# Kernel optimization log

Measured on AMD Instinct MI355X. Metric: run time of the kernel, lower is better.

The kernel has to match this reference:

```python
import jax, jax.numpy as jnp
import numpy as np

B, S, D, H, DQK, DV, DFF, L = 8, 512, 512, 8, 64, 64, 2048, 2
SCALE = float(np.sqrt(DQK))


def sinusoid_pe(s, d):
    pos = jnp.arange(s, dtype=jnp.float32)[:, None]
    div = jnp.exp(jnp.arange(0, d, 2, dtype=jnp.float32) * (-np.log(10000.0) / d))
    pe = jnp.zeros((s, d), jnp.float32)
    pe = pe.at[:, 0::2].set(jnp.sin(pos * div))
    pe = pe.at[:, 1::2].set(jnp.cos(pos * div))
    return pe


def ms_masks(s, steps=(4, 8, 16), rep=2):
    # Vectorized equivalent of multi_scale_mask: window of `step` neighbors,
    # shifted near the boundaries so the total neighbor count stays = step.
    i = jnp.arange(s)[:, None]
    j = jnp.arange(s)[None, :]
    ms = []
    for step in steps:
        s2 = step // 2
        left = jnp.where(i < s // 2, jnp.minimum(i, s2), step - jnp.minimum(s - 1 - i, s2))
        right = step - left
        m = (j >= i - left) & (j <= i + right)
        ms += [m] * rep
    return jnp.stack(ms)  # [6, S, S] bool


def layer_norm(x, g, b):
    mu = x.mean(-1, keepdims=True)
    var = ((x - mu) ** 2).mean(-1, keepdims=True)
    return (x - mu) / jnp.sqrt(var + 1e-6) * g + b


def mha(qin, kin, vin, wq, wk, wv, wo, g, b, mask):
    bq, lq, _ = qin.shape
    lk = kin.shape[1]
    q = (qin @ wq).reshape(bq, lq, H, DQK).transpose(0, 2, 1, 3)  # bhqd
    k = (kin @ wk).reshape(bq, lk, H, DQK).transpose(0, 2, 1, 3)
    v = (vin @ wv).reshape(bq, lk, H, DV).transpose(0, 2, 1, 3)
    scores = jnp.einsum('bhqd,bhkd->bhqk', q / SCALE, k)
    scores = jnp.where(mask, scores, jnp.float32(-1e9))
    p = jax.nn.softmax(scores, axis=-1)
    o = jnp.einsum('bhqk,bhkd->bhqd', p, v).transpose(0, 2, 1, 3).reshape(bq, lq, H * DV)
    return layer_norm(o @ wo + qin, g, b)


def ffn(x, w1, b1, w2, b2, g, bb):
    h = jax.nn.relu(x @ w1 + b1)
    return layer_norm(h @ w2 + b2 + x, g, bb)


def setup_inputs() -> dict:
    key = jax.random.key(0)
    ks = jax.random.split(key, 40)
    it = iter(range(40))
    d = {}
    d['src_seq'] = jax.random.normal(ks[next(it)], (B, S, D), jnp.float32)
    d['trg_seq'] = jax.random.normal(ks[next(it)], (B, S, D), jnp.float32)
    d['enc_pad_num'] = jax.random.randint(ks[next(it)], (B,), 0, 64)
    d['dec_pad_num'] = jax.random.randint(ks[next(it)], (B,), 0, 64)

    def w(shape):
        return jax.random.normal(ks[next(it)], shape, jnp.float32) * 0.02

    for p in ('e_wq', 'e_wk', 'e_wv'):
        d[p] = w((L, D, H * DQK))
    d['e_wo'] = w((L, H * DV, D))
    d['e_g1'] = jnp.ones((L, D)); d['e_b1'] = jnp.zeros((L, D))
    d['e_w1'] = w((L, D, DFF)); d['e_bb1'] = jnp.zeros((L, DFF))
    d['e_w2'] = w((L, DFF, D)); d['e_bb2'] = jnp.zeros((L, D))
    d['e_g2'] = jnp.ones((L, D)); d['e_b2'] = jnp.zeros((L, D))
    for p in ('d_swq', 'd_swk', 'd_swv'):
        d[p] = w((L, D, H * DQK))
    d['d_swo'] = w((L, H * DV, D))
    d['d_g1'] = jnp.ones((L, D)); d['d_b1'] = jnp.zeros((L, D))
    for p in ('d_cwq', 'd_cwk', 'd_cwv'):
        d[p] = w((L, D, H * DQK))
    d['d_cwo'] = w((L, H * DV, D))
    d['d_g2'] = jnp.ones((L, D)); d['d_b2'] = jnp.zeros((L, D))
    d['d_w1'] = w((L, D, DFF)); d['d_bb1'] = jnp.zeros((L, DFF))
    d['d_w2'] = w((L, DFF, D)); d['d_bb2'] = jnp.zeros((L, D))
    d['d_g3'] = jnp.ones((L, D)); d['d_b3'] = jnp.zeros((L, D))
    return d


def reference(src_seq, trg_seq, enc_pad_num, dec_pad_num,
              e_wq, e_wk, e_wv, e_wo, e_g1, e_b1, e_w1, e_bb1, e_w2, e_bb2, e_g2, e_b2,
              d_swq, d_swk, d_swv, d_swo, d_g1, d_b1,
              d_cwq, d_cwk, d_cwv, d_cwo, d_g2, d_b2,
              d_w1, d_bb1, d_w2, d_bb2, d_g3, d_b3):
    ms = ms_masks(S)  # [6, S, S]
    src_pad = jnp.arange(S)[None, :] < (S - enc_pad_num)[:, None]  # [B, S]
    trg_pad = jnp.arange(S)[None, :] < (S - dec_pad_num)[:, None]

    def full_mask(pad):
        base = pad[:, None, None, :]  # [B,1,1,S]
        win = jnp.logical_and(ms[None], base)  # [B,6,S,S]
        dense = jnp.broadcast_to(base, (B, H - ms.shape[0], S, S))
        return jnp.concatenate([win, dense], axis=1)  # [B,H,S,S]

    src_mask = full_mask(src_pad)
    trg_mask = full_mask(trg_pad)
    pe = sinusoid_pe(S, D)

    x = src_seq + pe[None]
    for l in range(L):
        x = mha(x, x, x, e_wq[l], e_wk[l], e_wv[l], e_wo[l], e_g1[l], e_b1[l], src_mask)
        x = ffn(x, e_w1[l], e_bb1[l], e_w2[l], e_bb2[l], e_g2[l], e_b2[l])

    y = trg_seq + pe[None]
    for l in range(L):
        y = mha(y, y, y, d_swq[l], d_swk[l], d_swv[l], d_swo[l], d_g1[l], d_b1[l], trg_mask)
        y = mha(y, x, x, d_cwq[l], d_cwk[l], d_cwv[l], d_cwo[l], d_g2[l], d_b2[l], src_mask)
        y = ffn(y, d_w1[l], d_bb1[l], d_w2[l], d_bb2[l], d_g3[l], d_b3[l])
    return y
```

## Files before the change

kernel.cpp:

```cpp
#include <hip/hip_runtime.h>
#include <hip/hip_bf16.h>

#define BB 8
#define SS 512
#define DD 512
#define HH 8
#define DQKv 64
#define DFFv 2048
#define LL 2

typedef __attribute__((ext_vector_type(8))) __bf16 bf16x8;
typedef __attribute__((ext_vector_type(4))) float f32x4;

static __device__ __forceinline__ ushort f2b(float x) {
    unsigned int u = __float_as_uint(x);
    unsigned int r = (u + 0x7FFFu + ((u >> 16) & 1u)) >> 16;
    return (ushort)r;
}
static __device__ __forceinline__ float b2f(ushort u) {
    return __uint_as_float(((unsigned int)u) << 16);
}

typedef __attribute__((address_space(1))) const unsigned int gas_u32;
typedef __attribute__((address_space(3))) unsigned int las_u32;
static __device__ __forceinline__ void gload16(const void* g, void* l) {
    __builtin_amdgcn_global_load_lds((gas_u32*)g, (las_u32*)l, 16, 0, 0);
}

#define VMCNT4 asm volatile("s_waitcnt vmcnt(4)" ::: "memory")
#define VMCNT6 asm volatile("s_waitcnt vmcnt(6)" ::: "memory")
#define VMCNT0 asm volatile("s_waitcnt vmcnt(0)" ::: "memory")
#define LGKM0  asm volatile("s_waitcnt lgkmcnt(0)" ::: "memory")
#define SCHEDB __builtin_amdgcn_sched_barrier(0)
#define SBAR   __builtin_amdgcn_s_barrier()

__global__ __launch_bounds__(256) void add_pe2_k(const float* __restrict__ src,
                                                 const float* __restrict__ trg,
                                                 float* __restrict__ xf,
                                                 ushort* __restrict__ xb,
                                                 float* __restrict__ yf,
                                                 ushort* __restrict__ yb) {
    const int NQ = BB * SS * DD / 4;
    int i = blockIdx.x * 256 + threadIdx.x;
    const bool second = i >= NQ;
    const int ii = second ? i - NQ : i;
    const int rem = ii & (SS * DD / 4 - 1);
    const int d4 = rem & (DD / 4 - 1);
    const int s = rem >> 7;

    float4 a = ((const float4*)(second ? trg : src))[ii];
    const float c = -9.210340371976184f / 512.0f;
    const float div0 = __expf((float)(4 * d4) * c);
    const float div1 = __expf((float)(4 * d4 + 2) * c);
    const float a0 = (float)s * div0, a1 = (float)s * div1;
    a.x += sinf(a0); a.y += cosf(a0);
    a.z += sinf(a1); a.w += cosf(a1);

    float* of = second ? yf : xf;
    ushort* ob = second ? yb : xb;
    ((float4*)of)[ii] = a;
    ushort4 ub;
    ub.x = f2b(a.x); ub.y = f2b(a.y); ub.z = f2b(a.z); ub.w = f2b(a.w);
    ((ushort4*)ob)[ii] = ub;
}

__global__ __launch_bounds__(256) void tcast_k(const float* __restrict__ s0,
                                               const float* __restrict__ s1,
                                               const float* __restrict__ s2,
                                               const float* __restrict__ s3,
                                               ushort* __restrict__ dst,
                                               int K, int N) {
    __shared__ ushort st[64][72];
    const float* src = (blockIdx.z == 0) ? s0 : (blockIdx.z == 1) ? s1
                     : (blockIdx.z == 2) ? s2 : s3;
    ushort* d = dst + (size_t)blockIdx.z * K * N;
    const int k0 = blockIdx.y * 64, n0 = blockIdx.x * 64;
    const int t = threadIdx.x;
    const int r = t >> 2, c4 = (t & 3) * 16;
#pragma unroll
    for (int i = 0; i < 16; i += 4) {
        float4 v = *(const float4*)&src[(size_t)(k0 + r) * N + n0 + c4 + i];
        st[c4 + i + 0][r] = f2b(v.x);
        st[c4 + i + 1][r] = f2b(v.y);
        st[c4 + i + 2][r] = f2b(v.z);
        st[c4 + i + 3][r] = f2b(v.w);
    }
    __syncthreads();
    const int n = t >> 2, seg = (t & 3) * 16;
    *(uint4*)&d[(size_t)(n0 + n) * K + k0 + seg]     = *(const uint4*)&st[n][seg];
    *(uint4*)&d[(size_t)(n0 + n) * K + k0 + seg + 8] = *(const uint4*)&st[n][seg + 8];
}

#define NW 32
struct WTab {
    const float* src[NW];
    unsigned off[NW];
    int Kd[NW];
    int Nd[NW];
    int cum[NW + 1];
};

__global__ __launch_bounds__(256) void tcast_all_k(WTab tab, ushort* __restrict__ dst) {
    __shared__ ushort st[64][72];
    const int t = blockIdx.x;
    int m = 0;
    while (t >= tab.cum[m + 1]) ++m;
    const int local = t - tab.cum[m];
    const int ntx = tab.Nd[m];
    const int bx = local % ntx, by = local / ntx;
    const float* src = tab.src[m];
    ushort* d = dst + tab.off[m];
    const int N = ntx * 64, K = tab.Kd[m] * 64;
    const int k0 = by * 64, n0 = bx * 64;

    const int tt = threadIdx.x;
    const int r = tt >> 2, c4 = (tt & 3) * 16;
#pragma unroll
    for (int i = 0; i < 16; i += 4) {
        float4 v = *(const float4*)&src[(size_t)(k0 + r) * N + n0 + c4 + i];
        st[c4 + i + 0][r] = f2b(v.x);
        st[c4 + i + 1][r] = f2b(v.y);
        st[c4 + i + 2][r] = f2b(v.z);
        st[c4 + i + 3][r] = f2b(v.w);
    }
    __syncthreads();
    const int n = tt >> 2, seg = (tt & 3) * 16;
    *(uint4*)&d[(size_t)(n0 + n) * K + k0 + seg]     = *(const uint4*)&st[n][seg];
    *(uint4*)&d[(size_t)(n0 + n) * K + k0 + seg + 8] = *(const uint4*)&st[n][seg + 8];
}

template <bool BIAS, bool RES, bool RELU, bool OUTBF>
__global__ __launch_bounds__(256) void gemm2_k(const ushort* __restrict__ A,
                                               const ushort* __restrict__ Bt,
                                               const float* __restrict__ bias,
                                               const float* __restrict__ res,
                                               void* __restrict__ Cout,
                                               int M, int N, int K, int nbx) {
    __shared__ ushort sA[3][64 * 64];
    __shared__ ushort sB[3][64 * 64];

    const int tid = threadIdx.x;
    const int nwg = gridDim.x;
    const int wg = blockIdx.x;
    const int swz = (wg & 7) * (nwg >> 3) + (wg >> 3);
    const int bx = swz % nbx, by = swz / nbx;

    const int lane = tid & 63, w = tid >> 6;
    const int wm = w >> 1, wn = w & 1;
    const int llo = lane & 15, lhi = lane >> 4;

    const int srow = tid >> 3;
    const int scol = (((tid & 7) ^ (srow & 7)) * 8);
    const ushort* Ab = A + (size_t)(by * 64 + srow) * K + scol;
    const ushort* Bb = Bt + (size_t)(bx * 64 + srow) * K + scol;
    const int sOff = srow * 128 + (tid & 7) * 16;

    f32x4 acc[2][2] = {};
    const int nt = K >> 6;

#pragma unroll
    for (int i = 0; i < 2; ++i) {
        gload16(Ab + (size_t)i * 32 * K, (char*)sA[0] + sOff + i * 32 * 128);
        gload16(Bb + (size_t)i * 32 * K, (char*)sB[0] + sOff + i * 32 * 128);
    }
    if (nt > 1) {
#pragma unroll
        for (int i = 0; i < 2; ++i) {
            gload16(Ab + (size_t)i * 32 * K + 64, (char*)sA[1] + sOff + i * 32 * 128);
            gload16(Bb + (size_t)i * 32 * K + 64, (char*)sB[1] + sOff + i * 32 * 128);
        }
    }
    SCHEDB;

    for (int t = 0; t < nt; ++t) {
        if (t + 1 < nt) { VMCNT4; } else { VMCNT0; }
        LGKM0;
        SCHEDB;
        SBAR;
        SCHEDB;
        if (t + 2 < nt) {
            const int k0 = (t + 2) << 6;
            char* dA = (char*)sA[(t + 2) % 3] + sOff;
            char* dB = (char*)sB[(t + 2) % 3] + sOff;
#pragma unroll
            for (int i = 0; i < 2; ++i) {
                gload16(Ab + (size_t)i * 32 * K + k0, dA + i * 32 * 128);
                gload16(Bb + (size_t)i * 32 * K + k0, dB + i * 32 * 128);
            }
        }
        SCHEDB;
        const ushort* cA = sA[t % 3];
        const ushort* cB = sB[t % 3];
        const int sw = llo & 7;
#pragma unroll
        for (int ks = 0; ks < 2; ++ks) {
            const int pc = ((ks * 4 + lhi) ^ sw) * 8;
            bf16x8 af[2];
#pragma unroll
            for (int fa = 0; fa < 2; ++fa)
                af[fa] = *(const bf16x8*)&cA[(wm * 32 + fa * 16 + llo) * 64 + pc];
            bf16x8 bfrag[2];
#pragma unroll
            for (int fb = 0; fb < 2; ++fb)
                bfrag[fb] = *(const bf16x8*)&cB[(wn * 32 + fb * 16 + llo) * 64 + pc];
#pragma unroll
            for (int fa = 0; fa < 2; ++fa)
#pragma unroll
                for (int fb = 0; fb < 2; ++fb)
                    acc[fa][fb] = __builtin_amdgcn_mfma_f32_16x16x32_bf16(
                        af[fa], bfrag[fb], acc[fa][fb], 0, 0, 0);
        }
    }

#pragma unroll
    for (int fa = 0; fa < 2; ++fa) {
#pragma unroll
        for (int fb = 0; fb < 2; ++fb) {
            const int col = bx * 64 + wn * 32 + fb * 16 + llo;
            const float bv = BIAS ? bias[col] : 0.f;
#pragma unroll
            for (int j = 0; j < 4; ++j) {
                const int row = by * 64 + wm * 32 + fa * 16 + lhi * 4 + j;
                float v = acc[fa][fb][j] + bv;
                if (RES) v += res[(size_t)row * N + col];
                if (RELU) v = fmaxf(v, 0.f);
                if (OUTBF) ((ushort*)Cout)[(size_t)row * N + col] = f2b(v);
                else       ((float*)Cout)[(size_t)row * N + col] = v;
            }
        }
    }
}

template <bool BIAS, bool RES, bool RELU, bool OUTBF>
__global__ __launch_bounds__(256) void gemm3_k(const ushort* __restrict__ A,
                                               const ushort* __restrict__ Bt,
                                               const float* __restrict__ bias,
                                               const float* __restrict__ res,
                                               void* __restrict__ Cout,
                                               int M, int N, int K, int nbx) {
    __shared__ ushort sA[2][64 * 64];
    __shared__ ushort sB[2][128 * 64];

    const int tid = threadIdx.x;
    const int nwg = gridDim.x;
    const int wg = blockIdx.x;
    const int swz = (wg & 7) * (nwg >> 3) + (wg >> 3);
    const int bx = swz % nbx, by = swz / nbx;

    const int lane = tid & 63, w = tid >> 6;
    const int wm = w >> 1, wn = w & 1;
    const int llo = lane & 15, lhi = lane >> 4;

    const int srow = tid >> 3;
    const int scol = (((tid & 7) ^ (srow & 7)) * 8);
    const ushort* Ab = A + (size_t)(by * 64 + srow) * K + scol;
    const ushort* Bb = Bt + (size_t)(bx * 128 + srow) * K + scol;
    const int sOff = srow * 128 + (tid & 7) * 16;

    f32x4 acc[2][4] = {};
    const int nt = K >> 6;

#pragma unroll
    for (int i = 0; i < 2; ++i)
        gload16(Ab + (size_t)i * 32 * K, (char*)sA[0] + sOff + i * 32 * 128);
#pragma unroll
    for (int i = 0; i < 4; ++i)
        gload16(Bb + (size_t)i * 32 * K, (char*)sB[0] + sOff + i * 32 * 128);
    SCHEDB;

    for (int t = 0; t < nt; ++t) {
        if (t + 1 < nt) {
            const int k0 = (t + 1) << 6;
            char* dA = (char*)sA[(t + 1) & 1] + sOff;
            char* dB = (char*)sB[(t + 1) & 1] + sOff;
#pragma unroll
            for (int i = 0; i < 2; ++i)
                gload16(Ab + (size_t)i * 32 * K + k0, dA + i * 32 * 128);
#pragma unroll
            for (int i = 0; i < 4; ++i)
                gload16(Bb + (size_t)i * 32 * K + k0, dB + i * 32 * 128);
            SCHEDB;
            VMCNT6;
        } else {
            VMCNT0;
        }
        SCHEDB;
        SBAR;
        SCHEDB;
        const ushort* cA = sA[t & 1];
        const ushort* cB = sB[t & 1];
        const int sw = llo & 7;
#pragma unroll
        for (int ks = 0; ks < 2; ++ks) {
            const int pc = ((ks * 4 + lhi) ^ sw) * 8;
            bf16x8 af[2];
#pragma unroll
            for (int fa = 0; fa < 2; ++fa)
                af[fa] = *(const bf16x8*)&cA[(wm * 32 + fa * 16 + llo) * 64 + pc];
            bf16x8 bfrag[4];
#pragma unroll
            for (int fb = 0; fb < 4; ++fb)
                bfrag[fb] = *(const bf16x8*)&cB[(wn * 64 + fb * 16 + llo) * 64 + pc];
#pragma unroll
            for (int fa = 0; fa < 2; ++fa)
#pragma unroll
                for (int fb = 0; fb < 4; ++fb)
                    acc[fa][fb] = __builtin_amdgcn_mfma_f32_16x16x32_bf16(
                        af[fa], bfrag[fb], acc[fa][fb], 0, 0, 0);
        }
        LGKM0;
        SCHEDB;
        SBAR;
    }

#pragma unroll
    for (int fa = 0; fa < 2; ++fa) {
#pragma unroll
        for (int fb = 0; fb < 4; ++fb) {
            const int col = bx * 128 + wn * 64 + fb * 16 + llo;
            const float bv = BIAS ? bias[col] : 0.f;
#pragma unroll
            for (int j = 0; j < 4; ++j) {
                const int row = by * 64 + wm * 32 + fa * 16 + lhi * 4 + j;
                float v = acc[fa][fb][j] + bv;
                if (RES) v += res[(size_t)row * N + col];
                if (RELU) v = fmaxf(v, 0.f);
                if (OUTBF) ((ushort*)Cout)[(size_t)row * N + col] = f2b(v);
                else       ((float*)Cout)[(size_t)row * N + col] = v;
            }
        }
    }
}

__global__ __launch_bounds__(256) void attn_k(const ushort* __restrict__ QKV,
                                              ushort* __restrict__ O,
                                              const int* __restrict__ pad) {
    __shared__ ushort sQ[64][72];
    __shared__ ushort sK[64][72];
    __shared__ ushort sVt[64][72];
    __shared__ ushort sP[64][72];

    const int tid = threadIdx.x;
    const int b = blockIdx.z, h = blockIdx.y, q0 = blockIdx.x << 6;
    const int klim = SS - pad[b];
    const int lane = tid & 63, w = tid >> 6;
    const int qw0 = w << 4;
    const int lhi = lane >> 4, llo = lane & 15;
    const int ST = 3 * DD;

    {
        const int r = tid >> 2, seg = (tid & 3) << 4;
        const ushort* src = &QKV[(size_t)(b * SS + q0 + r) * ST + h * DQKv + seg];
        *(uint4*)&sQ[r][seg]     = *(const uint4*)src;
        *(uint4*)&sQ[r][seg + 8] = *(const uint4*)(src + 8);
    }

    auto window = [&](int i, int& wlo, int& whi) {
        if (h < 6) {
            const int step = 4 << (h >> 1);
            const int s2 = step >> 1;
            const int a1 = (i < s2) ? i : s2;
            const int a2 = ((SS - 1 - i) < s2) ? (SS - 1 - i) : s2;
            const int left = (i < SS / 2) ? a1 : (step - a2);
            wlo = i - left;
            whi = wlo + step;
        } else {
            wlo = 0;
            whi = SS - 1;
        }
    };

    int lo[4], hi[4];
#pragma unroll
    for (int j = 0; j < 4; ++j) window(q0 + qw0 + lhi * 4 + j, lo[j], hi[j]);

    int kt0 = 0, kt1 = SS;
    if (h < 6) {
        int lo0, hi0, lo63, hi63;
        window(q0, lo0, hi0);
        window(q0 + 63, lo63, hi63);
        if (lo63 >= klim) {
            kt0 = 0; kt1 = SS;
        } else {
            kt0 = (lo0 >> 6) << 6;
            kt1 = ((hi63 >> 6) + 1) << 6;
            if (kt1 > SS) kt1 = SS;
        }
    }

    float mr[4] = {-1e30f, -1e30f, -1e30f, -1e30f};
    float lr[4] = {0.f, 0.f, 0.f, 0.f};
    f32x4 oacc[4] = {};

    for (int kt = kt0; kt < kt1; kt += 64) {
        __syncthreads();
        {
            const int r = tid >> 2, seg = (tid & 3) << 4;
            const ushort* ksrc = &QKV[(size_t)(b * SS + kt + r) * ST + DD + h * DQKv + seg];
            *(uint4*)&sK[r][seg]     = *(const uint4*)ksrc;
            *(uint4*)&sK[r][seg + 8] = *(const uint4*)(ksrc + 8);
            const ushort* vsrc = &QKV[(size_t)(b * SS + kt + r) * ST + 2 * DD + h * DQKv + seg];
            uint4 u0 = *(const uint4*)vsrc;
            uint4 u1 = *(const uint4*)(vsrc + 8);
            const ushort* v0 = (const ushort*)&u0;
            const ushort* v1 = (const ushort*)&u1;
#pragma unroll
            for (int i = 0; i < 8; ++i) sVt[seg + i][r] = v0[i];
#pragma unroll
            for (int i = 0; i < 8; ++i) sVt[seg + 8 + i][r] = v1[i];
        }
        __syncthreads();

        f32x4 sacc[4] = {};
#pragma unroll
        for (int ks = 0; ks < 2; ++ks) {
            bf16x8 aq = *(const bf16x8*)&sQ[qw0 + llo][ks * 32 + lhi * 8];
#pragma unroll
            for (int n = 0; n < 4; ++n) {
                bf16x8 bk = *(const bf16x8*)&sK[n * 16 + llo][ks * 32 + lhi * 8];
                sacc[n] = __builtin_amdgcn_mfma_f32_16x16x32_bf16(aq, bk, sacc[n], 0, 0, 0);
            }
        }

#pragma unroll
        for (int j = 0; j < 4; ++j) {
            float s[4];
#pragma unroll
            for (int n = 0; n < 4; ++n) {
                const int kidx = kt + n * 16 + llo;
                const bool ok = (kidx < klim) && (kidx >= lo[j]) && (kidx <= hi[j]);
                s[n] = ok ? (sacc[n][j] * 0.125f) : -1e9f;
            }
            float tm = fmaxf(fmaxf(s[0], s[1]), fmaxf(s[2], s[3]));
#pragma unroll
            for (int off = 8; off; off >>= 1) tm = fmaxf(tm, __shfl_xor(tm, off));
            const float mn = fmaxf(mr[j], tm);
            const float alpha = __expf(mr[j] - mn);
            mr[j] = mn;
            float ps = 0.f;
            const int prow = qw0 + lhi * 4 + j;
#pragma unroll
            for (int n = 0; n < 4; ++n) {
                const ushort pb = f2b(__expf(s[n] - mn));
                sP[prow][n * 16 + llo] = pb;
                ps += b2f(pb);
            }
#pragma unroll
            for (int off = 8; off; off >>= 1) ps += __shfl_xor(ps, off);
            lr[j] = lr[j] * alpha + ps;
            oacc[0][j] *= alpha; oacc[1][j] *= alpha;
            oacc[2][j] *= alpha; oacc[3][j] *= alpha;
        }

#pragma unroll
        for (int ks = 0; ks < 2; ++ks) {
            bf16x8 ap = *(const bf16x8*)&sP[qw0 + llo][ks * 32 + lhi * 8];
#pragma unroll
            for (int n = 0; n < 4; ++n) {
                bf16x8 bv = *(const bf16x8*)&sVt[n * 16 + llo][ks * 32 + lhi * 8];
                oacc[n] = __builtin_amdgcn_mfma_f32_16x16x32_bf16(ap, bv, oacc[n], 0, 0, 0);
            }
        }
    }

#pragma unroll
    for (int j = 0; j < 4; ++j) {
        const float inv = 1.f / lr[j];
        const int q = q0 + qw0 + lhi * 4 + j;
#pragma unroll
        for (int n = 0; n < 4; ++n) {
            O[(size_t)(b * SS + q) * (HH * DQKv) + h * DQKv + n * 16 + llo] =
                f2b(oacc[n][j] * inv);
        }
    }
}

__global__ __launch_bounds__(256) void ln_k(const float* __restrict__ in,
                                            const float* __restrict__ g,
                                            const float* __restrict__ bvec,
                                            float* __restrict__ outf,
                                            ushort* __restrict__ outb) {
    const int row = blockIdx.x;
    const int tid = threadIdx.x;
    const float2 xv = *(const float2*)&in[(size_t)row * DD + tid * 2];

    __shared__ float red[4];
    __shared__ float red2[4];
    const int wid = tid >> 6, lane = tid & 63;

    float s = xv.x + xv.y;
#pragma unroll
    for (int off = 32; off; off >>= 1) s += __shfl_xor(s, off);
    if (lane == 0) red[wid] = s;
    __syncthreads();
    const float mu = (red[0] + red[1] + red[2] + red[3]) * (1.f / 512.f);

    const float dx = xv.x - mu, dy = xv.y - mu;
    float q = dx * dx + dy * dy;
#pragma unroll
    for (int off = 32; off; off >>= 1) q += __shfl_xor(q, off);
    if (lane == 0) red2[wid] = q;
    __syncthreads();
    const float var = (red2[0] + red2[1] + red2[2] + red2[3]) * (1.f / 512.f);
    const float rs = rsqrtf(var + 1e-6f);

    float2 o;
    o.x = dx * rs * g[tid * 2] + bvec[tid * 2];
    o.y = dy * rs * g[tid * 2 + 1] + bvec[tid * 2 + 1];
    *(float2*)&outf[(size_t)row * DD + tid * 2] = o;
    ushort2 ub; ub.x = f2b(o.x); ub.y = f2b(o.y);
    *(ushort2*)&outb[(size_t)row * DD + tid * 2] = ub;
}

extern "C" void kernel_launch(void* const* d_in, const int* in_sizes, int n_in,
                              void* d_out, int out_size, void* d_ws, size_t ws_size,
                              hipStream_t stream) {
    const float* src_seq = (const float*)d_in[0];
    const float* trg_seq = (const float*)d_in[1];
    const int* enc_pad = (const int*)d_in[2];
    const int* dec_pad = (const int*)d_in[3];
    const float* e_wq = (const float*)d_in[4];
    const float* e_wk = (const float*)d_in[5];
    const float* e_wv = (const float*)d_in[6];
    const float* e_wo = (const float*)d_in[7];
    const float* e_g1 = (const float*)d_in[8];
    const float* e_b1 = (const float*)d_in[9];
    const float* e_w1 = (const float*)d_in[10];
    const float* e_bb1 = (const float*)d_in[11];
    const float* e_w2 = (const float*)d_in[12];
    const float* e_bb2 = (const float*)d_in[13];
    const float* e_g2 = (const float*)d_in[14];
    const float* e_b2 = (const float*)d_in[15];
    const float* d_swq = (const float*)d_in[16];
    const float* d_swk = (const float*)d_in[17];
    const float* d_swv = (const float*)d_in[18];
    const float* d_swo = (const float*)d_in[19];
    const float* d_g1 = (const float*)d_in[20];
    const float* d_b1 = (const float*)d_in[21];
    const float* d_cwq = (const float*)d_in[22];
    const float* d_cwk = (const float*)d_in[23];
    const float* d_cwv = (const float*)d_in[24];
    const float* d_cwo = (const float*)d_in[25];
    const float* d_g2 = (const float*)d_in[26];
    const float* d_b2 = (const float*)d_in[27];
    const float* d_w1 = (const float*)d_in[28];
    const float* d_bb1 = (const float*)d_in[29];
    const float* d_w2 = (const float*)d_in[30];
    const float* d_bb2 = (const float*)d_in[31];
    const float* d_g3 = (const float*)d_in[32];
    const float* d_b3 = (const float*)d_in[33];
    (void)in_sizes; (void)n_in; (void)out_size;

    const int M = BB * SS;
    const int NTOK = BB * SS * DD;
    const size_t WSZ = (size_t)DD * 512;

    float* ws = (float*)d_ws;
    float* x  = ws;
    float* y  = x + NTOK;
    float* t0 = y + NTOK;
    ushort* xbf  = (ushort*)(t0 + NTOK);
    ushort* ybf  = xbf + NTOK;
    ushort* qkvb = ybf + NTOK;
    ushort* ob   = qkvb + (size_t)M * 1536;
    ushort* hbf  = qkvb;
    ushort* warena = ob + NTOK;

    const float* wsrc[NW]; int wK[NW], wN[NW]; size_t woff[NW];
    int wcnt = 0; size_t acc = 0;
    auto push = [&](const float* p, int K, int N) {
        wsrc[wcnt] = p; wK[wcnt] = K; wN[wcnt] = N; woff[wcnt] = acc;
        acc += (size_t)K * N; ++wcnt;
    };
    for (int l = 0; l < LL; ++l) {
        push(e_wq + (size_t)l * WSZ, 512, 512);
        push(e_wk + (size_t)l * WSZ, 512, 512);
        push(e_wv + (size_t)l * WSZ, 512, 512);
        push(e_wo + (size_t)l * WSZ, 512, 512);
        push(e_w1 + (size_t)l * DD * DFFv, 512, DFFv);
        push(e_w2 + (size_t)l * DFFv * DD, DFFv, 512);
    }
    for (int l = 0; l < LL; ++l) {
        push(d_swq + (size_t)l * WSZ, 512, 512);
        push(d_swk + (size_t)l * WSZ, 512, 512);
        push(d_swv + (size_t)l * WSZ, 512, 512);
        push(d_swo + (size_t)l * WSZ, 512, 512);
        push(d_cwq + (size_t)l * WSZ, 512, 512);
        push(d_cwk + (size_t)l * WSZ, 512, 512);
        push(d_cwv + (size_t)l * WSZ, 512, 512);
        push(d_cwo + (size_t)l * WSZ, 512, 512);
        push(d_w1 + (size_t)l * DD * DFFv, 512, DFFv);
        push(d_w2 + (size_t)l * DFFv * DD, DFFv, 512);
    }

    const size_t base_bytes = (size_t)(warena - (ushort*)d_ws) * 2;
    const bool big = ws_size >= base_bytes + acc * 2;

    if (big) {
        WTab tab;
        int tiles = 0;
        for (int i = 0; i < NW; ++i) {
            tab.src[i] = wsrc[i];
            tab.off[i] = (unsigned)woff[i];
            tab.Kd[i] = wK[i] / 64;
            tab.Nd[i] = wN[i] / 64;
            tab.cum[i] = tiles;
            tiles += (wK[i] / 64) * (wN[i] / 64);
        }
        tab.cum[NW] = tiles;
        tcast_all_k<<<tiles, 256, 0, stream>>>(tab, warena);
    }

    add_pe2_k<<<2 * NTOK / 4 / 256, 256, 0, stream>>>(src_seq, trg_seq, x, xbf, y, ybf);

    auto do_mha = [&](float* statef, ushort* statebf, const ushort* kvbf, int widx,
                      const float* g, const float* bb, const int* pad) {
        const ushort* bt;
        if (big) {
            bt = warena + woff[widx];
        } else {
            tcast_k<<<dim3(8, 8, 4), 256, 0, stream>>>(
                wsrc[widx], wsrc[widx + 1], wsrc[widx + 2], wsrc[widx + 3],
                warena, 512, 512);
            bt = warena;
        }
        if (kvbf == statebf) {
            gemm3_k<false, false, false, true><<<64 * 12, 256, 0, stream>>>(
                statebf, bt, nullptr, nullptr, qkvb, M, 1536, 512, 12);
        } else {
            gemm2_k<false, false, false, true><<<64 * 8, 256, 0, stream>>>(
                statebf, bt + 0 * WSZ, nullptr, nullptr, qkvb, M, 1536, 512, 8);
            gemm3_k<false, false, false, true><<<64 * 8, 256, 0, stream>>>(
                kvbf, bt + 1 * WSZ, nullptr, nullptr, qkvb + DD, M, 1536, 512, 8);
        }
        attn_k<<<dim3(SS / 64, HH, BB), 256, 0, stream>>>(qkvb, ob, pad);
        gemm2_k<false, true, false, false><<<64 * 8, 256, 0, stream>>>(
            ob, bt + 3 * WSZ, nullptr, statef, t0, M, 512, 512, 8);
        ln_k<<<M, 256, 0, stream>>>(t0, g, bb, statef, statebf);
    };
    auto do_ffn = [&](float* statef, ushort* statebf, int widx,
                      const float* b1, const float* b2,
                      const float* g, const float* bb, float* lnoutf) {
        const ushort* bt1;
        const ushort* bt2;
        if (big) {
            bt1 = warena + woff[widx];
            bt2 = warena + woff[widx + 1];
        } else {
            tcast_k<<<dim3(32, 8, 1), 256, 0, stream>>>(
                wsrc[widx], wsrc[widx], wsrc[widx], wsrc[widx], warena, 512, DFFv);
            bt1 = warena;
            bt2 = warena;
        }
        gemm3_k<true, false, true, true><<<64 * 16, 256, 0, stream>>>(
            statebf, bt1, b1, nullptr, hbf, M, DFFv, 512, 16);
        if (!big) {
            tcast_k<<<dim3(8, 32, 1), 256, 0, stream>>>(
                wsrc[widx + 1], wsrc[widx + 1], wsrc[widx + 1], wsrc[widx + 1],
                warena, DFFv, 512);
        }
        gemm2_k<true, true, false, false><<<64 * 8, 256, 0, stream>>>(
            hbf, bt2, b2, statef, t0, M, 512, DFFv, 8);
        ln_k<<<M, 256, 0, stream>>>(t0, g, bb, lnoutf, statebf);
    };

    for (int l = 0; l < LL; ++l) {
        do_mha(x, xbf, xbf, l * 6, e_g1 + l * DD, e_b1 + l * DD, enc_pad);
        do_ffn(x, xbf, l * 6 + 4, e_bb1 + l * DFFv, e_bb2 + l * DD,
               e_g2 + l * DD, e_b2 + l * DD, x);
    }
    for (int l = 0; l < LL; ++l) {
        do_mha(y, ybf, ybf, 12 + l * 10, d_g1 + l * DD, d_b1 + l * DD, dec_pad);
        do_mha(y, ybf, xbf, 12 + l * 10 + 4, d_g2 + l * DD, d_b2 + l * DD, enc_pad);
        const bool last = (l == LL - 1);
        do_ffn(y, ybf, 12 + l * 10 + 8, d_bb1 + l * DFFv, d_bb2 + l * DD,
               d_g3 + l * DD, d_b3 + l * DD, last ? (float*)d_out : y);
    }
}
```

Baseline: 588.2 us.

## Drop fp32 residual stream, split-K FFN down-projection with fused reduce+LayerNorm

The fp32 copies of the encoder and decoder states are removed, so residual adds read the bf16 state and LayerNorm writes only bf16, except for the final output. The FFN second GEMM (K=2048) becomes a split-K kernel that writes two fp32 partials, and a new LN kernel sums them with bias and residual before normalising. This cuts memory traffic and raises the workgroup count for the long-K GEMM, at the cost of extra partial-sum traffic. The residual path now carries bf16 rounding, which lowers accuracy.

Measured after the change: 550.8 us. 6.4% less time.

```diff
diff --git a/kernel.cpp b/kernel.cpp
--- a/kernel.cpp
+++ b/kernel.cpp
@@ -36,9 +36,7 @@
 
 __global__ __launch_bounds__(256) void add_pe2_k(const float* __restrict__ src,
                                                  const float* __restrict__ trg,
-                                                 float* __restrict__ xf,
                                                  ushort* __restrict__ xb,
-                                                 float* __restrict__ yf,
                                                  ushort* __restrict__ yb) {
     const int NQ = BB * SS * DD / 4;
     int i = blockIdx.x * 256 + threadIdx.x;
@@ -56,9 +54,7 @@
     a.x += sinf(a0); a.y += cosf(a0);
     a.z += sinf(a1); a.w += cosf(a1);
 
-    float* of = second ? yf : xf;
     ushort* ob = second ? yb : xb;
-    ((float4*)of)[ii] = a;
     ushort4 ub;
     ub.x = f2b(a.x); ub.y = f2b(a.y); ub.z = f2b(a.z); ub.w = f2b(a.w);
     ((ushort4*)ob)[ii] = ub;
@@ -133,7 +129,7 @@
 __global__ __launch_bounds__(256) void gemm2_k(const ushort* __restrict__ A,
                                                const ushort* __restrict__ Bt,
                                                const float* __restrict__ bias,
-                                               const float* __restrict__ res,
+                                               const ushort* __restrict__ res,
                                                void* __restrict__ Cout,
                                                int M, int N, int K, int nbx) {
     __shared__ ushort sA[3][64 * 64];
@@ -222,7 +218,7 @@
             for (int j = 0; j < 4; ++j) {
                 const int row = by * 64 + wm * 32 + fa * 16 + lhi * 4 + j;
                 float v = acc[fa][fb][j] + bv;
-                if (RES) v += res[(size_t)row * N + col];
+                if (RES) v += b2f(res[(size_t)row * N + col]);
                 if (RELU) v = fmaxf(v, 0.f);
                 if (OUTBF) ((ushort*)Cout)[(size_t)row * N + col] = f2b(v);
                 else       ((float*)Cout)[(size_t)row * N + col] = v;
@@ -231,11 +227,110 @@
     }
 }
 
+__global__ __launch_bounds__(256) void gemm2s_k(const ushort* __restrict__ A,
+                                                const ushort* __restrict__ Bt,
+                                                float* __restrict__ P0,
+                                                float* __restrict__ P1,
+                                                int M, int N, int K) {
+    __shared__ ushort sA[3][64 * 64];
+    __shared__ ushort sB[3][64 * 64];
+
+    const int tid = threadIdx.x;
+    const int nwg = gridDim.x;
+    const int wg = blockIdx.x;
+    const int swz = (wg & 7) * (nwg >> 3) + (wg >> 3);
+    const int bx = swz & 7;
+    const int r2 = swz >> 3;
+    const int by = r2 & 63;
+    const int kh = r2 >> 6;
+    const int Kh = K >> 1;
+    const int kbase = kh * Kh;
+
+    const int lane = tid & 63, w = tid >> 6;
+    const int wm = w >> 1, wn = w & 1;
+    const int llo = lane & 15, lhi = lane >> 4;
+
+    const int srow = tid >> 3;
+    const int scol = (((tid & 7) ^ (srow & 7)) * 8);
+    const ushort* Ab = A + (size_t)(by * 64 + srow) * K + kbase + scol;
+    const ushort* Bb = Bt + (size_t)(bx * 64 + srow) * K + kbase + scol;
+    const int sOff = srow * 128 + (tid & 7) * 16;
+
+    f32x4 acc[2][2] = {};
+    const int nt = Kh >> 6;
+
+#pragma unroll
+    for (int i = 0; i < 2; ++i) {
+        gload16(Ab + (size_t)i * 32 * K, (char*)sA[0] + sOff + i * 32 * 128);
+        gload16(Bb + (size_t)i * 32 * K, (char*)sB[0] + sOff + i * 32 * 128);
+    }
+#pragma unroll
+    for (int i = 0; i < 2; ++i) {
+        gload16(Ab + (size_t)i * 32 * K + 64, (char*)sA[1] + sOff + i * 32 * 128);
+        gload16(Bb + (size_t)i * 32 * K + 64, (char*)sB[1] + sOff + i * 32 * 128);
+    }
+    SCHEDB;
+
+    for (int t = 0; t < nt; ++t) {
+        if (t + 1 < nt) { VMCNT4; } else { VMCNT0; }
+        LGKM0;
+        SCHEDB;
+        SBAR;
+        SCHEDB;
+        if (t + 2 < nt) {
+            const int k0 = (t + 2) << 6;
+            char* dA = (char*)sA[(t + 2) % 3] + sOff;
+            char* dB = (char*)sB[(t + 2) % 3] + sOff;
+#pragma unroll
+            for (int i = 0; i < 2; ++i) {
+                gload16(Ab + (size_t)i * 32 * K + k0, dA + i * 32 * 128);
+                gload16(Bb + (size_t)i * 32 * K + k0, dB + i * 32 * 128);
+            }
+        }
+        SCHEDB;
+        const ushort* cA = sA[t % 3];
+        const ushort* cB = sB[t % 3];
+        const int sw = llo & 7;
+#pragma unroll
+        for (int ks = 0; ks < 2; ++ks) {
+            const int pc = ((ks * 4 + lhi) ^ sw) * 8;
+            bf16x8 af[2];
+#pragma unroll
+            for (int fa = 0; fa < 2; ++fa)
+                af[fa] = *(const bf16x8*)&cA[(wm * 32 + fa * 16 + llo) * 64 + pc];
+            bf16x8 bfrag[2];
+#pragma unroll
+            for (int fb = 0; fb < 2; ++fb)
+                bfrag[fb] = *(const bf16x8*)&cB[(wn * 32 + fb * 16 + llo) * 64 + pc];
+#pragma unroll
+            for (int fa = 0; fa < 2; ++fa)
+#pragma unroll
+                for (int fb = 0; fb < 2; ++fb)
+                    acc[fa][fb] = __builtin_amdgcn_mfma_f32_16x16x32_bf16(
+                        af[fa], bfrag[fb], acc[fa][fb], 0, 0, 0);
+        }
+    }
+
+    float* P = kh ? P1 : P0;
+#pragma unroll
+    for (int fa = 0; fa < 2; ++fa) {
+#pragma unroll
+        for (int fb = 0; fb < 2; ++fb) {
+            const int col = bx * 64 + wn * 32 + fb * 16 + llo;
+#pragma unroll
+            for (int j = 0; j < 4; ++j) {
+                const int row = by * 64 + wm * 32 + fa * 16 + lhi * 4 + j;
+                P[(size_t)row * N + col] = acc[fa][fb][j];
+            }
+        }
+    }
+}
+
 template <bool BIAS, bool RES, bool RELU, bool OUTBF>
 __global__ __launch_bounds__(256) void gemm3_k(const ushort* __restrict__ A,
                                                const ushort* __restrict__ Bt,
                                                const float* __restrict__ bias,
-                                               const float* __restrict__ res,
+                                               const ushort* __restrict__ res,
                                                void* __restrict__ Cout,
                                                int M, int N, int K, int nbx) {
     __shared__ ushort sA[2][64 * 64];
@@ -323,7 +418,7 @@
             for (int j = 0; j < 4; ++j) {
                 const int row = by * 64 + wm * 32 + fa * 16 + lhi * 4 + j;
                 float v = acc[fa][fb][j] + bv;
-                if (RES) v += res[(size_t)row * N + col];
+                if (RES) v += b2f(res[(size_t)row * N + col]);
                 if (RELU) v = fmaxf(v, 0.f);
                 if (OUTBF) ((ushort*)Cout)[(size_t)row * N + col] = f2b(v);
                 else       ((float*)Cout)[(size_t)row * N + col] = v;
@@ -478,8 +573,8 @@
 __global__ __launch_bounds__(256) void ln_k(const float* __restrict__ in,
                                             const float* __restrict__ g,
                                             const float* __restrict__ bvec,
-                                            float* __restrict__ outf,
-                                            ushort* __restrict__ outb) {
+                                            ushort* __restrict__ outb,
+                                            float* __restrict__ outf) {
     const int row = blockIdx.x;
     const int tid = threadIdx.x;
     const float2 xv = *(const float2*)&in[(size_t)row * DD + tid * 2];
@@ -507,9 +602,55 @@
     float2 o;
     o.x = dx * rs * g[tid * 2] + bvec[tid * 2];
     o.y = dy * rs * g[tid * 2 + 1] + bvec[tid * 2 + 1];
-    *(float2*)&outf[(size_t)row * DD + tid * 2] = o;
     ushort2 ub; ub.x = f2b(o.x); ub.y = f2b(o.y);
     *(ushort2*)&outb[(size_t)row * DD + tid * 2] = ub;
+    if (outf) *(float2*)&outf[(size_t)row * DD + tid * 2] = o;
+}
+
+__global__ __launch_bounds__(256) void ln2_k(const float* __restrict__ p0,
+                                             const float* __restrict__ p1,
+                                             const float* __restrict__ bias,
+                                             const ushort* __restrict__ res,
+                                             const float* __restrict__ g,
+                                             const float* __restrict__ bvec,
+                                             ushort* __restrict__ outb,
+                                             float* __restrict__ outf) {
+    const int row = blockIdx.x;
+    const int tid = threadIdx.x;
+    const size_t base = (size_t)row * DD + tid * 2;
+    const float2 a0 = *(const float2*)&p0[base];
+    const float2 a1 = *(const float2*)&p1[base];
+    const ushort2 rv = *(const ushort2*)&res[base];
+    float2 xv;
+    xv.x = a0.x + a1.x + bias[tid * 2]     + b2f(rv.x);
+    xv.y = a0.y + a1.y + bias[tid * 2 + 1] + b2f(rv.y);
+
+    __shared__ float red[4];
+    __shared__ float red2[4];
+    const int wid = tid >> 6, lane = tid & 63;
+
+    float s = xv.x + xv.y;
+#pragma unroll
+    for (int off = 32; off; off >>= 1) s += __shfl_xor(s, off);
+    if (lane == 0) red[wid] = s;
+    __syncthreads();
+    const float mu = (red[0] + red[1] + red[2] + red[3]) * (1.f / 512.f);
+
+    const float dx = xv.x - mu, dy = xv.y - mu;
+    float q = dx * dx + dy * dy;
+#pragma unroll
+    for (int off = 32; off; off >>= 1) q += __shfl_xor(q, off);
+    if (lane == 0) red2[wid] = q;
+    __syncthreads();
+    const float var = (red2[0] + red2[1] + red2[2] + red2[3]) * (1.f / 512.f);
+    const float rs = rsqrtf(var + 1e-6f);
+
+    float2 o;
+    o.x = dx * rs * g[tid * 2] + bvec[tid * 2];
+    o.y = dy * rs * g[tid * 2 + 1] + bvec[tid * 2 + 1];
+    ushort2 ub; ub.x = f2b(o.x); ub.y = f2b(o.y);
+    *(ushort2*)&outb[base] = ub;
+    if (outf) *(float2*)&outf[base] = o;
 }
 
 extern "C" void kernel_launch(void* const* d_in, const int* in_sizes, int n_in,
@@ -556,10 +697,10 @@
     const size_t WSZ = (size_t)DD * 512;
 
     float* ws = (float*)d_ws;
-    float* x  = ws;
-    float* y  = x + NTOK;
-    float* t0 = y + NTOK;
-    ushort* xbf  = (ushort*)(t0 + NTOK);
+    float* t0 = ws;
+    float* p0 = t0 + NTOK;
+    float* p1 = p0 + NTOK;
+    ushort* xbf  = (ushort*)(p1 + NTOK);
     ushort* ybf  = xbf + NTOK;
     ushort* qkvb = ybf + NTOK;
     ushort* ob   = qkvb + (size_t)M * 1536;
@@ -593,7 +734,7 @@
         push(d_w2 + (size_t)l * DFFv * DD, DFFv, 512);
     }
 
-    const size_t base_bytes = (size_t)(warena - (ushort*)d_ws) * 2;
+    const size_t base_bytes = (size_t)((char*)warena - (char*)d_ws);
     const bool big = ws_size >= base_bytes + acc * 2;
 
     if (big) {
@@ -611,9 +752,9 @@
         tcast_all_k<<<tiles, 256, 0, stream>>>(tab, warena);
     }
 
-    add_pe2_k<<<2 * NTOK / 4 / 256, 256, 0, stream>>>(src_seq, trg_seq, x, xbf, y, ybf);
-
-    auto do_mha = [&](float* statef, ushort* statebf, const ushort* kvbf, int widx,
+    add_pe2_k<<<2 * NTOK / 4 / 256, 256, 0, stream>>>(src_seq, trg_seq, xbf, ybf);
+
+    auto do_mha = [&](ushort* statebf, const ushort* kvbf, int widx,
                       const float* g, const float* bb, const int* pad) {
         const ushort* bt;
         if (big) {
@@ -635,10 +776,10 @@
         }
         attn_k<<<dim3(SS / 64, HH, BB), 256, 0, stream>>>(qkvb, ob, pad);
         gemm2_k<false, true, false, false><<<64 * 8, 256, 0, stream>>>(
-            ob, bt + 3 * WSZ, nullptr, statef, t0, M, 512, 512, 8);
-        ln_k<<<M, 256, 0, stream>>>(t0, g, bb, statef, statebf);
+            ob, bt + 3 * WSZ, nullptr, statebf, t0, M, 512, 512, 8);
+        ln_k<<<M, 256, 0, stream>>>(t0, g, bb, statebf, nullptr);
     };
-    auto do_ffn = [&](float* statef, ushort* statebf, int widx,
+    auto do_ffn = [&](ushort* statebf, int widx,
                       const float* b1, const float* b2,
                       const float* g, const float* bb, float* lnoutf) {
         const ushort* bt1;
@@ -659,21 +800,20 @@
                 wsrc[widx + 1], wsrc[widx + 1], wsrc[widx + 1], wsrc[widx + 1],
                 warena, DFFv, 512);
         }
-        gemm2_k<true, true, false, false><<<64 * 8, 256, 0, stream>>>(
-            hbf, bt2, b2, statef, t0, M, 512, DFFv, 8);
-        ln_k<<<M, 256, 0, stream>>>(t0, g, bb, lnoutf, statebf);
+        gemm2s_k<<<1024, 256, 0, stream>>>(hbf, bt2, p0, p1, M, 512, DFFv);
+        ln2_k<<<M, 256, 0, stream>>>(p0, p1, b2, statebf, g, bb, statebf, lnoutf);
     };
 
     for (int l = 0; l < LL; ++l) {
-        do_mha(x, xbf, xbf, l * 6, e_g1 + l * DD, e_b1 + l * DD, enc_pad);
-        do_ffn(x, xbf, l * 6 + 4, e_bb1 + l * DFFv, e_bb2 + l * DD,
-               e_g2 + l * DD, e_b2 + l * DD, x);
+        do_mha(xbf, xbf, l * 6, e_g1 + l * DD, e_b1 + l * DD, enc_pad);
+        do_ffn(xbf, l * 6 + 4, e_bb1 + l * DFFv, e_bb2 + l * DD,
+               e_g2 + l * DD, e_b2 + l * DD, nullptr);
     }
     for (int l = 0; l < LL; ++l) {
-        do_mha(y, ybf, ybf, 12 + l * 10, d_g1 + l * DD, d_b1 + l * DD, dec_pad);
-        do_mha(y, ybf, xbf, 12 + l * 10 + 4, d_g2 + l * DD, d_b2 + l * DD, enc_pad);
+        do_mha(ybf, ybf, 12 + l * 10, d_g1 + l * DD, d_b1 + l * DD, dec_pad);
+        do_mha(ybf, xbf, 12 + l * 10 + 4, d_g2 + l * DD, d_b2 + l * DD, enc_pad);
         const bool last = (l == LL - 1);
-        do_ffn(y, ybf, 12 + l * 10 + 8, d_bb1 + l * DFFv, d_bb2 + l * DD,
-               d_g3 + l * DD, d_b3 + l * DD, last ? (float*)d_out : y);
-    }
-}
+        do_ffn(ybf, 12 + l * 10 + 8, d_bb1 + l * DFFv, d_bb2 + l * DD,
+               d_g3 + l * DD, d_b3 + l * DD, last ? (float*)d_out : nullptr);
+    }
+}
```
